# Performance work log

Hardware: AMD Instinct MI355X
Metric: run time of the kernel (lower is better)

## Reference

```python
import jax, jax.numpy as jnp
import numpy as np

B, N, F, L = 16, 1536, 128, 2   # batch, input_features, enc(=dec)_features, n_layers
SLOPE = 0.2                      # LeakyReLU alpha
NEG = -1e9                       # mask fill for softmax


def setup_inputs() -> dict:
    key = jax.random.key(0)
    ks = jax.random.split(key, 14)
    g = lambda k, shape, s=0.05: (jax.random.normal(k, shape, jnp.float32) * s)
    data = jax.random.randint(ks[0], (B, N), 0, 2)          # binary presence vector
    embed = g(ks[1], (N + 1, F)).at[0].set(0.0)              # padding_idx=0 row zeroed
    return {
        "data": data,
        "embed": embed,
        "enc_W": g(ks[2], (L, F, F)),
        "enc_a_src": g(ks[3], (L, F)),
        "enc_a_dst": g(ks[4], (L, F)),
        "param_W": g(ks[5], (F, 2 * F)),
        "param_b": g(ks[6], (2 * F,)),
        "dec_W": g(ks[7], (F, F)),
        "dec_a_src": g(ks[8], (F,)),
        "dec_a_dst": g(ks[9], (F,)),
        "out_W1": g(ks[10], (F, F)),
        "out_b1": g(ks[11], (F,)),
        "out_W2": g(ks[12], (F, 1)),
        "out_b2": g(ks[13], (1,)),
    }


def _gat(x, mask, W, a_src, a_dst):
    """Single-head graph attention over a dense boolean adjacency `mask`.
    Equivalent to sparse GAT over the clique edge list data_to_edges() builds
    (self-loops included). Rows with no edges output 0."""
    h = x @ W                                    # (n, F)
    si = h @ a_src                               # (n,)
    sj = h @ a_dst                               # (n,)
    e = jax.nn.leaky_relu(si[:, None] + sj[None, :], SLOPE)
    e = jnp.where(mask, e, NEG)
    attn = jax.nn.softmax(e, axis=-1) * mask.any(axis=-1)[:, None]
    return attn @ h                              # (n, F)


def reference(data, embed, enc_W, enc_a_src, enc_a_dst, param_W, param_b,
              dec_W, dec_a_src, dec_a_dst, out_W1, out_b1, out_W2, out_b2):
    def per_sample(g):
        d = g != 0                               # active feature nodes
        m_in = d[:, None] & d[None, :]           # input clique adjacency (N, N)
        x = embed[:-1]                           # node features = embedding rows (N, F)
        for l in range(L):                       # encoder layers (n_layers=2)
            x = jax.nn.elu(_gat(x, m_in, enc_W[l], enc_a_src[l], enc_a_dst[l]))
        # variational parameterization (eval mode: dropout=id, reparam -> mean)
        par = x @ param_W + param_b              # (N, 2F)
        mean, sigma = par[:, :F], par[:, F:]
        w = (g == 1).astype(mean.dtype)
        cnt = jnp.maximum(w.sum(), 1.0)
        kld = 0.5 * jnp.sum(w[:, None] * (jnp.exp(sigma) - sigma - 1.0 + mean ** 2)) / cnt
        # append master node (last embedding row) and decode over extended clique
        enc_full = jnp.concatenate([mean, embed[-1:]], axis=0)      # (N+1, F)
        d_ext = jnp.concatenate([d, jnp.ones((1,), bool)])
        m_out = d_ext[:, None] & d_ext[None, :]                     # (N+1, N+1)
        dec = jax.nn.relu(_gat(enc_full, m_out, dec_W, dec_a_src, dec_a_dst))
        return dec[-1], kld                      # master-node readout (F,)

    feats, klds = jax.vmap(per_sample)(data)     # (B, F), (B,)
    pred = jax.nn.relu(feats @ out_W1 + out_b1) @ out_W2 + out_b2   # (B, 1)
    return pred, jnp.sum(klds)
```

## Files before the change

### kernel.cpp

```cpp
#include <hip/hip_runtime.h>

#define BB 16
#define NN 1536
#define FF 128
#define SLOPE 0.2f
#define NS 2048
#define CH2 32
#define NCH2 48
#define TI 8
#define NPB (NN/8)
#define DCS 64
#define NDC 24

__global__ __launch_bounds__(1024) void k_sortpre(
    const int* __restrict__ data,
    const float* __restrict__ embed, const float* __restrict__ decW,
    const float* __restrict__ aS, const float* __restrict__ aD,
    const float* __restrict__ SJb, long sStride,
    int* __restrict__ actG, int* __restrict__ cntG,
    float* __restrict__ hN, float* __restrict__ sN,
    float* __restrict__ keyG, int* __restrict__ pjG,
    float* __restrict__ SBG, float* __restrict__ SDG)
{
  int b = blockIdx.x, t = threadIdx.x;
  if (b == BB){
    __shared__ float rs[2][2];
    if (t < FF){
      float acc = 0.f;
      for (int k=0;k<FF;++k) acc += embed[(long)NN*FF + k] * decW[k*FF + t];
      hN[t] = acc;
      float ps = acc * aS[t];
      float pd = acc * aD[t];
      #pragma unroll
      for (int o=32;o;o>>=1){ ps += __shfl_down(ps,o); pd += __shfl_down(pd,o); }
      if ((t&63)==0){ rs[0][t>>6]=ps; rs[1][t>>6]=pd; }
    }
    __syncthreads();
    if (t==0){ sN[0]=rs[0][0]+rs[0][1]; sN[1]=rs[1][0]+rs[1][1]; }
    return;
  }

  __shared__ float key[NS]; __shared__ int pj[NS];
  __shared__ float sb[NS]; __shared__ float sd[NS];
  __shared__ int cntS;
  int cnt;
  if (data != nullptr){
    __shared__ int s[256];
    const int PER = NN/256;
    int local[NN/256]; int nl = 0;
    if (t < 256){
      int base = t*PER;
      #pragma unroll
      for (int u=0; u<PER; ++u){
        if (data[b*NN + base + u] != 0) local[nl++] = base+u;
      }
      s[t]=nl;
    }
    __syncthreads();
    if (t==0){ int run=0; for (int i=0;i<256;i++){ int v=s[i]; s[i]=run; run+=v; }
               cntG[b]=run; cntS=run; }
    __syncthreads();
    if (t < 256){
      int o = s[t];
      for (int u=0; u<nl; ++u) actG[b*NN + o + u] = local[u];
    }
    __syncthreads();
    cnt = cntS;
  } else {
    cnt = cntG[b];
  }

  const float* SJ = SJb + (long)b*sStride;
  const int* act = (data != nullptr) ? actG + b*NN : nullptr;
  int NSort = 32; while (NSort < cnt) NSort <<= 1;

  for (int e=t; e<NSort; e+=1024){
    if (e<cnt){ int io = act ? act[e] : e; key[e]=SJ[io]; pj[e]=io; }
    else { key[e]=__builtin_inff(); pj[e]=0; }
  }
  __syncthreads();
  for (int k=2; k<=NSort; k<<=1){
    for (int j=k>>1; j>0; j>>=1){
      for (int e=t; e<NSort; e+=1024){
        int l = e ^ j;
        if (l > e){
          bool asc = ((e & k) == 0);
          float a0=key[e], a1=key[l];
          if (asc ? (a0>a1) : (a0<a1)){
            key[e]=a1; key[l]=a0; int p=pj[e]; pj[e]=pj[l]; pj[l]=p;
          }
        }
      }
      __syncthreads();
    }
  }
  for (int e=t; e<NSort; e+=1024){
    if (e<cnt){ float kk=key[e]; sb[e]=__expf(kk); sd[e]=__expf(SLOPE*kk); }
    else { sb[e]=0.f; sd[e]=0.f; }
  }
  __syncthreads();
  for (int off=1; off<NSort; off<<=1){
    float t0[2], t1[2]; int ne=0;
    for (int e=t; e<NSort; e+=1024){
      t0[ne] = (e>=off) ? sb[e-off] : 0.f;
      t1[ne] = (e>=off) ? sd[e-off] : 0.f;
      ne++;
    }
    __syncthreads();
    ne=0;
    for (int e=t; e<NSort; e+=1024){ sb[e]+=t0[ne]; sd[e]+=t1[ne]; ne++; }
    __syncthreads();
  }
  for (int e=t; e<cnt; e+=1024){
    keyG[(long)b*NN+e]=key[e]; pjG[(long)b*NN+e]=pj[e];
    SBG[(long)b*NN+e]=sb[e];   SDG[(long)b*NN+e]=sd[e];
  }
}

__global__ __launch_bounds__(128) void k_rowmm(const float* __restrict__ Xv,
    const float* __restrict__ W, const float* __restrict__ aS, const float* __restrict__ aD,
    float* __restrict__ H, float* __restrict__ SI, float* __restrict__ SJ)
{
  int r0 = blockIdx.x*8;
  int f = threadIdx.x;
  __shared__ float xs[8][FF];
  #pragma unroll
  for (int r=0;r<8;++r) xs[r][f] = Xv[(long)(r0+r)*FF + f];
  __syncthreads();
  float acc[8]={0.f,0.f,0.f,0.f,0.f,0.f,0.f,0.f};
  for (int k=0;k<FF;++k){
    float w = W[k*FF + f];
    #pragma unroll
    for (int r=0;r<8;++r) acc[r] += xs[r][k]*w;
  }
  float as = aS[f], ad = aD[f];
  __shared__ float red[2][8][2];
  #pragma unroll
  for (int r=0;r<8;++r){
    H[(long)(r0+r)*FF + f] = acc[r];
    float ps = acc[r]*as, pd = acc[r]*ad;
    #pragma unroll
    for (int o=32;o;o>>=1){ ps += __shfl_down(ps,o); pd += __shfl_down(pd,o); }
    if ((f&63)==0){ red[0][r][f>>6]=ps; red[1][r][f>>6]=pd; }
  }
  __syncthreads();
  if (f<8){
    SI[r0+f]=red[0][f][0]+red[0][f][1]; SJ[r0+f]=red[1][f][0]+red[1][f][1];
  }
}

__global__ __launch_bounds__(128) void k_chunk(
    const float* __restrict__ keyG, const int* __restrict__ pjG,
    const int* __restrict__ cntArr,
    const float* __restrict__ Hb, long hStride,
    float* __restrict__ PP, float* __restrict__ PM)
{
  int b = blockIdx.y, c = blockIdx.x, f = threadIdx.x;
  int cnt = cntArr[b];
  int k0 = c*CH2;
  if (k0 >= cnt) return;
  int k1 = k0+CH2; if (k1 > cnt) k1 = cnt;
  int kn = k1-k0;
  const float* H = Hb + (long)b*hStride + f;
  __shared__ int pjs[CH2]; __shared__ float wbs[CH2], wds[CH2];
  if (f < CH2 && f < kn){
    float kk = keyG[(long)b*NN + k0 + f];
    pjs[f] = pjG[(long)b*NN + k0 + f];
    wbs[f] = __expf(kk);
    wds[f] = __expf(SLOPE*kk);
  }
  __syncthreads();
  float accB=0.f, accD=0.f;
  float hbuf[8];
  #pragma unroll
  for (int i=0;i<8;i++) hbuf[i] = (i<kn) ? H[(long)pjs[i]*FF] : 0.f;
  long obase = ((long)b*NN + k0)*FF + f;
  int k=0;
  for (; k+8<=kn; k+=8){
    #pragma unroll
    for (int u=0;u<8;u++){
      float hv = hbuf[u];
      int kp = k+u+8;
      hbuf[u] = (kp<kn) ? H[(long)pjs[kp]*FF] : 0.f;
      accB = fmaf(wbs[k+u], hv, accB);
      accD = fmaf(wds[k+u], hv, accD);
      PP[obase + (long)(k+u)*FF] = accB;
      PM[obase + (long)(k+u)*FF] = accD;
    }
  }
  for (; k<kn; ++k){
    float hv = H[(long)pjs[k]*FF];
    accB = fmaf(wbs[k], hv, accB);
    accD = fmaf(wds[k], hv, accD);
    PP[obase + (long)k*FF] = accB;
    PM[obase + (long)k*FF] = accD;
  }
}

__global__ __launch_bounds__(128) void k_offs(
    const float* __restrict__ PP, const float* __restrict__ PM,
    const int* __restrict__ cntArr,
    float* __restrict__ OFB, float* __restrict__ OFD)
{
  int b = blockIdx.x, f = threadIdx.x;
  int cnt = cntArr[b];
  float rb=0.f, rd=0.f;
  long base = (long)b*(NCH2+1)*FF + f;
  for (int c=0;c<NCH2;++c){
    OFB[base + (long)c*FF] = rb;
    OFD[base + (long)c*FF] = rd;
    int k0 = c*CH2;
    if (k0 < cnt){
      int kend = k0+CH2; if (kend > cnt) kend = cnt; kend -= 1;
      rb += PP[((long)b*NN+kend)*FF+f];
      rd += PM[((long)b*NN+kend)*FF+f];
    }
  }
  OFB[base + (long)NCH2*FF] = rb;
  OFD[base + (long)NCH2*FF] = rd;
}

__global__ __launch_bounds__(128) void k_aggout_mm(
    const float* __restrict__ keyG, const float* __restrict__ SBG, const float* __restrict__ SDG,
    const float* __restrict__ PP, const float* __restrict__ PM,
    const float* __restrict__ OFB, const float* __restrict__ OFD,
    const float* __restrict__ SI1, const int* __restrict__ actB,
    const int* __restrict__ cntArr,
    const float* __restrict__ W, const float* __restrict__ aS, const float* __restrict__ aD,
    float* __restrict__ Hout, float* __restrict__ SIo, float* __restrict__ SJo)
{
  int b = blockIdx.y;
  int cnt = cntArr[b];
  int r0 = blockIdx.x*TI;
  if (r0 >= cnt) return;
  int f = threadIdx.x;
  const int* act = actB + b*NN;
  __shared__ float keys[NN];
  __shared__ int kk[TI]; __shared__ float sis[TI];
  __shared__ float xs2[TI][FF];

  for (int e=f; e<cnt; e+=128) keys[e] = keyG[(long)b*NN + e];
  __syncthreads();
  if (f < TI){
    int r = r0 + f;
    float si=0.f; int k=0;
    if (r < cnt){
      si = SI1[act[r]];
      float th = -si;
      int lo=0, hi=cnt;
      while (lo<hi){ int mid=(lo+hi)>>1; if (keys[mid]<=th) lo=mid+1; else hi=mid; }
      k = lo;
    }
    kk[f]=k; sis[f]=si;
  }
  __syncthreads();
  const float* ofb = OFB + (long)b*(NCH2+1)*FF;
  const float* ofd = OFD + (long)b*(NCH2+1)*FF;
  float TB  = ofb[(long)NCH2*FF + f];
  float TBs = SBG[(long)b*NN + (cnt-1)];
  int rmax = cnt - r0; if (rmax > TI) rmax = TI;
  for (int r=0; r<TI; ++r){
    float v = 0.f;
    if (r < rmax){
      int k = kk[r]; float si = sis[r];
      float PB=0.f, PD=0.f, SBv=0.f, SDv=0.f;
      if (k > 0){
        int c = (k-1)/CH2;
        PB = PP[((long)b*NN+(k-1))*FF+f] + ofb[(long)c*FF+f];
        PD = PM[((long)b*NN+(k-1))*FF+f] + ofd[(long)c*FF+f];
        SBv = SBG[(long)b*NN+(k-1)];
        SDv = SDG[(long)b*NN+(k-1)];
      }
      float ai=__expf(si), ci=__expf(SLOPE*si);
      float num = ai*(TB -PB ) + ci*PD;
      float den = ai*(TBs-SBv) + ci*SDv;
      float o2 = num/den;
      v = (o2>0.f)? o2 : (__expf(o2)-1.f);
    }
    xs2[r][f] = v;
  }
  __syncthreads();
  float acc2[TI];
  #pragma unroll
  for (int u=0;u<TI;++u) acc2[u]=0.f;
  for (int k=0;k<FF;k+=4){
    float w0 = W[(k  )*FF + f];
    float w1 = W[(k+1)*FF + f];
    float w2 = W[(k+2)*FF + f];
    float w3 = W[(k+3)*FF + f];
    #pragma unroll
    for (int u=0;u<TI;++u){
      float4 x = *reinterpret_cast<const float4*>(&xs2[u][k]);
      acc2[u] = fmaf(x.x,w0, fmaf(x.y,w1, fmaf(x.z,w2, fmaf(x.w,w3, acc2[u]))));
    }
  }
  float as = aS[f], ad = aD[f];
  __shared__ float red[2][TI][2];
  #pragma unroll
  for (int u=0;u<TI;++u){
    int rr=r0+u;
    if (rr<cnt) Hout[((long)b*NN+rr)*FF+f] = acc2[u];
    float ps = acc2[u]*as, pd = acc2[u]*ad;
    #pragma unroll
    for (int o=32;o;o>>=1){ ps += __shfl_down(ps,o); pd += __shfl_down(pd,o); }
    if ((f&63)==0){ red[0][u][f>>6]=ps; red[1][u][f>>6]=pd; }
  }
  __syncthreads();
  if (f < TI){
    int rr=r0+f;
    if (rr<cnt){
      SIo[(long)b*NN+rr]=red[0][f][0]+red[0][f][1];
      SJo[(long)b*NN+rr]=red[1][f][0]+red[1][f][1];
    }
  }
}

__global__ __launch_bounds__(128) void k_aggout(
    const float* __restrict__ keyG, const float* __restrict__ SBG, const float* __restrict__ SDG,
    const float* __restrict__ PP, const float* __restrict__ PM,
    const float* __restrict__ OFB, const float* __restrict__ OFD,
    const float* __restrict__ SIb,
    const int* __restrict__ cntArr, float* __restrict__ XoB)
{
  int b = blockIdx.y;
  int cnt = cntArr[b];
  int r0 = blockIdx.x*TI;
  if (r0 >= cnt) return;
  int f = threadIdx.x;
  const float* SI = SIb + (long)b*NN;
  float* xo = XoB + (long)b*NN*FF;
  __shared__ float keys[NN];
  __shared__ int kk[TI]; __shared__ float sis[TI];

  for (int e=f; e<cnt; e+=128) keys[e] = keyG[(long)b*NN + e];
  __syncthreads();
  if (f < TI){
    int r = r0 + f;
    float si=0.f; int k=0;
    if (r < cnt){
      si = SI[r];
      float th = -si;
      int lo=0, hi=cnt;
      while (lo<hi){ int mid=(lo+hi)>>1; if (keys[mid]<=th) lo=mid+1; else hi=mid; }
      k = lo;
    }
    kk[f]=k; sis[f]=si;
  }
  __syncthreads();
  const float* ofb = OFB + (long)b*(NCH2+1)*FF;
  const float* ofd = OFD + (long)b*(NCH2+1)*FF;
  float TB  = ofb[(long)NCH2*FF + f];
  float TBs = SBG[(long)b*NN + (cnt-1)];
  int rmax = cnt - r0; if (rmax > TI) rmax = TI;
  for (int r=0; r<rmax; ++r){
    int k = kk[r]; float si = sis[r];
    float PB=0.f, PD=0.f, SBv=0.f, SDv=0.f;
    if (k > 0){
      int c = (k-1)/CH2;
      PB = PP[((long)b*NN+(k-1))*FF+f] + ofb[(long)c*FF+f];
      PD = PM[((long)b*NN+(k-1))*FF+f] + ofd[(long)c*FF+f];
      SBv = SBG[(long)b*NN+(k-1)];
      SDv = SDG[(long)b*NN+(k-1)];
    }
    float ai=__expf(si), ci=__expf(SLOPE*si);
    float num = ai*(TB -PB ) + ci*PD;
    float den = ai*(TBs-SBv) + ci*SDv;
    float o2 = num/den;
    xo[(long)(r0+r)*FF + f] = (o2>0.f)? o2 : (__expf(o2)-1.f);
  }
}

__global__ __launch_bounds__(256) void k_pardec(const float* __restrict__ XC,
    const float* __restrict__ pW, const float* __restrict__ pB,
    const float* __restrict__ decW, const float* __restrict__ dAd,
    float* __restrict__ KPART, float* __restrict__ H3, float* __restrict__ SJd,
    const int* __restrict__ cntArr)
{
  int b = blockIdx.y; int cnt = cntArr[b];
  int bx = blockIdx.x;
  int r0 = bx*8;
  int t = threadIdx.x;
  if (r0>=cnt){
    if (t==0) KPART[b*NPB + bx] = 0.f;
    return;
  }
  const float* X = XC + (long)b*NN*FF;
  __shared__ float xs[8][FF];
  for (int e=t; e<8*FF; e+=256){
    int r=e>>7, k=e&127; int rr=r0+r;
    xs[r][k] = (rr<cnt) ? X[(long)rr*FF+k] : 0.f;
  }
  __syncthreads();
  float acc[8]={0.f,0.f,0.f,0.f,0.f,0.f,0.f,0.f};
  for (int k=0;k<FF;++k){
    float w = pW[k*2*FF + t];
    #pragma unroll
    for (int r=0;r<8;++r) acc[r]+=xs[r][k]*w;
  }
  float bb = pB[t];
  float kacc=0.f;
  #pragma unroll
  for (int r=0;r<8;++r){
    int rr=r0+r;
    if (rr>=cnt) continue;
    float v = acc[r]+bb;
    if (t<FF) kacc += v*v;
    else kacc += __expf(v)-v-1.f;
  }
  #pragma unroll
  for (int o=32;o;o>>=1) kacc += __shfl_down(kacc,o);
  __shared__ float rw[4];
  if ((t&63)==0) rw[t>>6]=kacc;
  __syncthreads();
  if (t==0) KPART[b*NPB + bx] = rw[0]+rw[1]+rw[2]+rw[3];
  __shared__ float ms[8][FF];
  if (t < FF){
    #pragma unroll
    for (int r=0;r<8;++r){
      int rr=r0+r;
      ms[r][t] = (rr<cnt) ? acc[r]+bb : 0.f;
    }
  }
  __syncthreads();
  int h = t>>7, f = t&127;
  float a2[4]={0.f,0.f,0.f,0.f};
  for (int k=0;k<FF;++k){
    float w = decW[k*FF + f];
    #pragma unroll
    for (int u=0;u<4;++u) a2[u] += ms[h*4+u][k]*w;
  }
  float ad = dAd[f];
  __shared__ float redD[8][2];
  #pragma unroll
  for (int u=0;u<4;++u){
    int rq = h*4+u; int rr = r0+rq;
    if (rr<cnt) H3[((long)b*NN+rr)*FF+f] = a2[u];
    float pd = a2[u]*ad;
    #pragma unroll
    for (int o=32;o;o>>=1) pd += __shfl_down(pd,o);
    if ((t&63)==0) redD[rq][(t>>6)&1]=pd;
  }
  __syncthreads();
  if (t<8){
    int rr=r0+t;
    if (rr<cnt) SJd[(long)b*NN+rr]=redD[t][0]+redD[t][1];
  }
}

__global__ __launch_bounds__(128) void k_dec(const float* __restrict__ H3,
    const float* __restrict__ SJ3, const float* __restrict__ sN,
    const int* __restrict__ cntArr, float* __restrict__ DECP)
{
  int b=blockIdx.y, ch=blockIdx.x;
  int cnt=cntArr[b];
  int f=threadIdx.x;
  int r0=ch*DCS; int r1 = (r0+DCS < cnt) ? r0+DCS : cnt;
  float siN = sN[0];
  const float* H = H3 + (long)b*NN*FF;
  const float* SJ = SJ3 + (long)b*NN;
  float accV=0.f, accW=0.f;
  for (int r=r0;r<r1;++r){
    float sj=SJ[r]; float x=siN+sj;
    float e=(x>=0.f)? x : SLOPE*x;
    float w=__expf(e);
    accV += w*H[(long)r*FF+f];
    accW += w;
  }
  float* P = DECP + (long)(b*NDC+ch)*(FF+1);
  P[f]=accV;
  if (f==0) P[FF]=accW;
}

__global__ __launch_bounds__(128) void k_head(const float* __restrict__ DECP,
    const float* __restrict__ hN, const float* __restrict__ sN,
    const float* __restrict__ KPART, const int* __restrict__ cntArr,
    const float* __restrict__ W1, const float* __restrict__ b1,
    const float* __restrict__ W2, const float* __restrict__ b2,
    float* __restrict__ out)
{
  int b = blockIdx.x;
  int f = threadIdx.x;
  __shared__ float rw[2];
  if (b < BB){
    float siN=sN[0], sjN=sN[1];
    float xN=siN+sjN; float eN=(xN>=0.f)?xN:SLOPE*xN; float wN=__expf(eN);
    float num=0.f, den=0.f;
    for (int c=0;c<NDC;++c){
      const float* P = DECP + (long)(b*NDC+c)*(FF+1);
      num += P[f]; den += P[FF];
    }
    num += wN*hN[f]; den += wN;
    float v = num/den;
    __shared__ float feats[FF];
    feats[f] = (v>0.f)? v : 0.f;
    __syncthreads();
    float acc=0.f;
    for (int k=0;k<FF;++k) acc += feats[k]*W1[k*FF+f];
    acc += b1[f];
    acc = (acc>0.f)? acc : 0.f;
    float p = acc*W2[f];
    #pragma unroll
    for (int o=32;o;o>>=1) p += __shfl_down(p,o);
    if ((f&63)==0) rw[f>>6]=p;
    __syncthreads();
    if (f==0) out[b] = rw[0]+rw[1]+b2[0];
  } else {
    float s=0.f;
    for (int bb=0;bb<BB;++bb){
      float part=0.f;
      for (int c=f;c<NPB;c+=128) part += KPART[bb*NPB + c];
      #pragma unroll
      for (int o=32;o;o>>=1) part += __shfl_down(part,o);
      if ((f&63)==0) rw[f>>6]=part;
      __syncthreads();
      float tot = rw[0]+rw[1];
      int c=cntArr[bb]; float cf = (c>0)? (float)c : 1.f;
      s += 0.5f*tot/cf;
      __syncthreads();
    }
    if (f==0) out[16]=s;
  }
}

extern "C" void kernel_launch(void* const* d_in, const int* in_sizes, int n_in,
                              void* d_out, int out_size, void* d_ws, size_t ws_size,
                              hipStream_t stream)
{
  const int*   data  = (const int*)d_in[0];
  const float* embed = (const float*)d_in[1];
  const float* encW  = (const float*)d_in[2];
  const float* encAs = (const float*)d_in[3];
  const float* encAd = (const float*)d_in[4];
  const float* pW    = (const float*)d_in[5];
  const float* pB    = (const float*)d_in[6];
  const float* decW  = (const float*)d_in[7];
  const float* decAs = (const float*)d_in[8];
  const float* decAd = (const float*)d_in[9];
  const float* oW1   = (const float*)d_in[10];
  const float* oB1   = (const float*)d_in[11];
  const float* oW2   = (const float*)d_in[12];
  const float* oB2   = (const float*)d_in[13];
  float* out = (float*)d_out;

  float* w = (float*)d_ws;
  long o = 0;
  float* H1   = w+o; o += (long)NN*FF;
  float* H2   = w+o; o += (long)BB*NN*FF;
  float* XC   = w+o; o += (long)BB*NN*FF;
  float* PP   = w+o; o += (long)BB*NN*FF;
  float* PM   = w+o; o += (long)BB*NN*FF;
  float* SI1  = w+o; o += NN;
  float* SJ1  = w+o; o += NN;
  float* SI2  = w+o; o += (long)BB*NN;
  float* SJ2  = w+o; o += (long)BB*NN;
  float* KPART= w+o; o += (long)BB*NPB;
  float* hN   = w+o; o += FF;
  float* sN   = w+o; o += 2;
  float* DECP = w+o; o += (long)BB*NDC*(FF+1);
  float* keyG = w+o; o += (long)BB*NN;
  float* SBG  = w+o; o += (long)BB*NN;
  float* SDG  = w+o; o += (long)BB*NN;
  float* OFB  = w+o; o += (long)BB*(NCH2+1)*FF;
  float* OFD  = w+o; o += (long)BB*(NCH2+1)*FF;
  int* act = (int*)(w+o); o += (long)BB*NN;
  int* pjG = (int*)(w+o); o += (long)BB*NN;
  int* cnt = (int*)(w+o); o += BB;
  (void)in_sizes; (void)n_in; (void)out_size; (void)ws_size;

  k_rowmm<<<NN/8,128,0,stream>>>(embed, encW, encAs, encAd, H1, SI1, SJ1);
  k_sortpre<<<BB+1,1024,0,stream>>>(data, embed, decW, decAs, decAd,
      SJ1, 0L, act, cnt, hN, sN, keyG, pjG, SBG, SDG);
  k_chunk<<<dim3(NCH2,BB),128,0,stream>>>(keyG, pjG, cnt, H1, 0L, PP, PM);
  k_offs<<<BB,128,0,stream>>>(PP, PM, cnt, OFB, OFD);
  k_aggout_mm<<<dim3(NN/TI,BB),128,0,stream>>>(keyG, SBG, SDG, PP, PM, OFB, OFD,
      SI1, act, cnt, encW + FF*FF, encAs + FF, encAd + FF, H2, SI2, SJ2);
  k_sortpre<<<BB,1024,0,stream>>>(nullptr, embed, decW, decAs, decAd,
      SJ2, (long)NN, act, cnt, hN, sN, keyG, pjG, SBG, SDG);
  k_chunk<<<dim3(NCH2,BB),128,0,stream>>>(keyG, pjG, cnt, H2, (long)NN*FF, PP, PM);
  k_offs<<<BB,128,0,stream>>>(PP, PM, cnt, OFB, OFD);
  k_aggout<<<dim3(NN/TI,BB),128,0,stream>>>(keyG, SBG, SDG, PP, PM, OFB, OFD,
      SI2, cnt, XC);
  k_pardec<<<dim3(NPB,BB),256,0,stream>>>(XC, pW, pB, decW, decAd,
      KPART, H2 , SJ2 , cnt);
  k_dec<<<dim3(NDC,BB),128,0,stream>>>(H2 , SJ2, sN, cnt, DECP);
  k_head<<<BB+1,128,0,stream>>>(DECP, hN, sN, KPART, cnt, oW1, oB1, oW2, oB2, out);
}
```

Before: 278.2 us.

## Use wavefront shuffles for small bitonic stages and prefix-sum scan

The bitonic sort's inner stages with stride below 64 now run in registers via cross-lane xor shuffles inside one wavefront, not through shared memory with a barrier per step. The Hillis-Steele inclusive scan, which needed two barriers per offset, becomes a two-level scan: each thread sums two elements, does an intra-wave shuffle scan, then adds per-wave offsets. Both are meant to cut barrier count and LDS traffic in the per-batch sort/prefix kernel. The shuffle stage relies on 64-lane wavefronts and NSort ≤ 2048.

```diff
diff --git a/kernel.cpp b/kernel.cpp
--- a/kernel.cpp
+++ b/kernel.cpp
@@ -79,8 +79,9 @@
     else { key[e]=__builtin_inff(); pj[e]=0; }
   }
   __syncthreads();
+
   for (int k=2; k<=NSort; k<<=1){
-    for (int j=k>>1; j>0; j>>=1){
+    for (int j=k>>1; j>=64; j>>=1){
       for (int e=t; e<NSort; e+=1024){
         int l = e ^ j;
         if (l > e){
@@ -93,24 +94,57 @@
       }
       __syncthreads();
     }
-  }
-  for (int e=t; e<NSort; e+=1024){
-    if (e<cnt){ float kk=key[e]; sb[e]=__expf(kk); sd[e]=__expf(SLOPE*kk); }
-    else { sb[e]=0.f; sd[e]=0.f; }
-  }
-  __syncthreads();
-  for (int off=1; off<NSort; off<<=1){
-    float t0[2], t1[2]; int ne=0;
-    for (int e=t; e<NSort; e+=1024){
-      t0[ne] = (e>=off) ? sb[e-off] : 0.f;
-      t1[ne] = (e>=off) ? sd[e-off] : 0.f;
-      ne++;
-    }
-    __syncthreads();
-    ne=0;
-    for (int e=t; e<NSort; e+=1024){ sb[e]+=t0[ne]; sd[e]+=t1[ne]; ne++; }
-    __syncthreads();
-  }
+    {
+      float v0=0.f, v1=0.f; int q0=0, q1=0;
+      if (t < NSort){ v0=key[t]; q0=pj[t]; }
+      if (NSort > 1024){ v1=key[t+1024]; q1=pj[t+1024]; }
+      int jstart = ((k>>1) < 32) ? (k>>1) : 32;
+      for (int j=jstart; j>0; j>>=1){
+        {
+          float ov=__shfl_xor(v0,j); int oq=__shfl_xor(q0,j);
+          bool keepmin = (((t & k)==0) == ((t & j)==0));
+          bool take = keepmin ? (ov < v0) : (ov > v0);
+          if (take){ v0=ov; q0=oq; }
+        }
+        if (NSort > 1024){
+          int e = t+1024;
+          float ov=__shfl_xor(v1,j); int oq=__shfl_xor(q1,j);
+          bool keepmin = (((e & k)==0) == ((e & j)==0));
+          bool take = keepmin ? (ov < v1) : (ov > v1);
+          if (take){ v1=ov; q1=oq; }
+        }
+      }
+      if (t < NSort){ key[t]=v0; pj[t]=q0; }
+      if (NSort > 1024){ key[t+1024]=v1; pj[t+1024]=q1; }
+    }
+    __syncthreads();
+  }
+
+  {
+    int e0 = 2*t, e1 = 2*t+1;
+    float b0=0.f,b1=0.f,d0=0.f,d1=0.f;
+    if (e0 < cnt){ float kk=key[e0]; b0=__expf(kk); d0=__expf(SLOPE*kk); }
+    if (e1 < cnt){ float kk=key[e1]; b1=__expf(kk); d1=__expf(SLOPE*kk); }
+    float sB=b0+b1, sD=d0+d1;
+    int lane = t & 63, wid = t >> 6;
+    float iB=sB, iD=sD;
+    #pragma unroll
+    for (int o=1;o<64;o<<=1){
+      float uB=__shfl_up(iB,o), uD=__shfl_up(iD,o);
+      if (lane>=o){ iB+=uB; iD+=uD; }
+    }
+    __shared__ float wsB[16], wsD[16];
+    if (lane==63){ wsB[wid]=iB; wsD[wid]=iD; }
+    __syncthreads();
+    float offB=0.f, offD=0.f;
+    for (int w=0; w<wid; ++w){ offB+=wsB[w]; offD+=wsD[w]; }
+    float exB = offB + iB - sB;
+    float exD = offD + iD - sD;
+    if (e0 < NSort){ sb[e0]=exB+b0;    sd[e0]=exD+d0; }
+    if (e1 < NSort){ sb[e1]=exB+b0+b1; sd[e1]=exD+d0+d1; }
+  }
+  __syncthreads();
+
   for (int e=t; e<cnt; e+=1024){
     keyG[(long)b*NN+e]=key[e]; pjG[(long)b*NN+e]=pj[e];
     SBG[(long)b*NN+e]=sb[e];   SDG[(long)b*NN+e]=sd[e];
```

Result: faster. 263.4 us (-5.3%).
